# Optimization experiments

Hardware: AMD Instinct MI355X
Metric: run time of the kernel (lower is better)

The kernel has to match this reference:

```python
import jax, jax.numpy as jnp
import numpy as np
from jax import lax

B, L, DIM = 2, 2048, 2048
HK, HV = 16, 32
DK, DV = 128, 128
KCONV = 4
KEY_DIM = HK * DK          # 2048
VAL_DIM = HV * DV          # 4096
CONV_DIM = 2 * KEY_DIM + VAL_DIM  # 8192
EPS = 1e-6


def _l2norm(x, eps=1e-6):
    return x * lax.rsqrt((x * x).sum(-1, keepdims=True) + eps)


def _gated_delta_rule(q, k, v, g, beta):
    # q,k: (B,L,H,DK); v: (B,L,H,DV); g,beta: (B,L,H)
    q = _l2norm(q.astype(jnp.float32)) * (DK ** -0.5)
    k = _l2norm(k.astype(jnp.float32))
    v = v.astype(jnp.float32)
    g = g.astype(jnp.float32)
    beta = beta.astype(jnp.float32)
    # time-major for scan: (L,B,H,...)
    qs = q.transpose(1, 0, 2, 3)
    ks = k.transpose(1, 0, 2, 3)
    vs = v.transpose(1, 0, 2, 3)
    gs = g.transpose(1, 0, 2)
    bs = beta.transpose(1, 0, 2)
    state0 = jnp.zeros((B, HV, DK, DV), jnp.float32)

    def step(state, inp):
        q_t, k_t, v_t, g_t, b_t = inp
        state = state * jnp.exp(g_t)[..., None, None]          # decay
        kv_mem = jnp.einsum('bhk,bhkv->bhv', k_t, state)       # read
        delta = (v_t - kv_mem) * b_t[..., None]                # error-correct
        state = state + jnp.einsum('bhk,bhv->bhkv', k_t, delta)
        out_t = jnp.einsum('bhk,bhkv->bhv', q_t, state)
        return state, out_t

    _, outs = lax.scan(step, state0, (qs, ks, vs, gs, bs))
    return outs.transpose(1, 0, 2, 3)  # (B,L,H,DV)


def setup_inputs() -> dict:
    key = jax.random.key(0)
    ks = jax.random.split(key, 8)
    s = 0.02
    return {
        'x': jax.random.normal(ks[0], (B, L, DIM), jnp.float32),
        'W_qkv': jax.random.normal(ks[1], (CONV_DIM, DIM), jnp.float32) * s,
        'W_z': jax.random.normal(ks[2], (VAL_DIM, DIM), jnp.float32) * s,
        'W_a': jax.random.normal(ks[3], (HV, DIM), jnp.float32) * s,
        'W_b': jax.random.normal(ks[4], (HV, DIM), jnp.float32) * s,
        'conv_w': jax.random.normal(ks[5], (CONV_DIM, 1, KCONV), jnp.float32) * 0.2,
        'A_log': jnp.log(jax.random.uniform(ks[6], (HV,), jnp.float32, 1e-6, 16.0)),
        'dt_bias': jnp.ones((HV,), jnp.float32),
        'norm_weight': jnp.ones((DV,), jnp.float32),
        'W_out': jax.random.normal(ks[7], (DIM, VAL_DIM), jnp.float32) * s,
    }


def reference(x, W_qkv, W_z, W_a, W_b, conv_w, A_log, dt_bias, norm_weight, W_out):
    qkv = x @ W_qkv.T                      # (B,L,CONV_DIM)
    z = x @ W_z.T                          # (B,L,VAL_DIM)
    a = x @ W_a.T                          # (B,L,HV)
    b = x @ W_b.T                          # (B,L,HV)
    # depthwise causal conv1d (left pad K-1)
    h = qkv.transpose(0, 2, 1)             # (B,C,L)
    h = lax.conv_general_dilated(h, conv_w, window_strides=(1,),
                                 padding=[(KCONV - 1, 0)],
                                 dimension_numbers=('NCH', 'OIH', 'NCH'),
                                 feature_group_count=CONV_DIM)
    qkv = jax.nn.silu(h.transpose(0, 2, 1))
    q, k, v = jnp.split(qkv, [KEY_DIM, 2 * KEY_DIM], axis=-1)
    q = q.reshape(B, L, HK, DK)
    k = k.reshape(B, L, HK, DK)
    v = v.reshape(B, L, HV, DV)
    rep = HV // HK
    if rep > 1:
        q = jnp.repeat(q, rep, axis=2)
        k = jnp.repeat(k, rep, axis=2)
    g = -jnp.exp(A_log.astype(jnp.float32)) * jax.nn.softplus(a.astype(jnp.float32) + dt_bias)
    beta = jax.nn.sigmoid(b)
    out = _gated_delta_rule(q, k, v, g, beta)   # (B,L,HV,DV) fp32
    # gated RMSNorm over DV: silu(z) * weight * norm(out)
    var = (out * out).mean(-1, keepdims=True)
    out = out * lax.rsqrt(var + EPS) * norm_weight
    zg = z.reshape(B, L, HV, DV)
    out = out * jax.nn.silu(zg.astype(jnp.float32))
    out = out.astype(x.dtype).reshape(B, L, VAL_DIM)
    return out @ W_out.T
```

## Files before the change

### kernel.cpp

```cpp
#include <hip/hip_runtime.h>
#include <hip/hip_bf16.h>
#include <cstddef>
#include <cstdint>

constexpr int B = 2, L = 2048, DIM = 2048;
constexpr int HK = 16, HV = 32, DK = 128, DV = 128;
constexpr int KEY_DIM = HK * DK;
constexpr int VAL_DIM = HV * DV;
constexpr int CONV_DIM = 2 * KEY_DIM + VAL_DIM;
constexpr int NPROJ = CONV_DIM + VAL_DIM + HV + HV;
constexpr int NPAD  = ((NPROJ + 255) / 256) * 256;
constexpr size_t ROWS = (size_t)B * L;
constexpr float EPS = 1e-6f;
constexpr int CHUNK = 64, NCHUNK = L / CHUNK;
constexpr int NCH_TOT = B * HV * NCHUNK;
constexpr int CONV_LT = 8;
constexpr int CONV_TL = L / CONV_LT;

constexpr size_t OFF_QKV  = 0;
constexpr size_t OFF_Z    = OFF_QKV + ROWS * CONV_DIM * 2;
constexpr size_t OFF_A    = OFF_Z   + ROWS * VAL_DIM * 2;
constexpr size_t OFF_B    = OFF_A   + ROWS * HV * 4;
constexpr size_t OFF_G    = OFF_B   + ROWS * HV * 4;
constexpr size_t OFF_BETA = OFF_G   + ROWS * HV * 4;
constexpr size_t OFF_U    = OFF_BETA + ROWS * HV * 4;
constexpr size_t OFF_WQK  = OFF_U + (size_t)NCH_TOT * CHUNK * DV * 4;
constexpr size_t OFF_HALO = OFF_WQK + (size_t)NCH_TOT * CHUNK * CHUNK * 2;
constexpr size_t WS_NEED_BYTES = OFF_HALO + (size_t)3 * B * CONV_LT * CONV_DIM * 2;
constexpr size_t OFF_WCAT = OFF_U;
constexpr size_t OFF_XB   = OFF_WQK;
constexpr size_t OFF_WOB  = OFF_U;
static_assert((size_t)NPAD * DIM * 2 <= (size_t)NCH_TOT * CHUNK * DV * 4, "Wcat fits U");

__device__ __forceinline__ float bf2f(unsigned short u) {
    union { float f; uint32_t i; } c; c.i = ((uint32_t)u) << 16; return c.f;
}
__device__ __forceinline__ unsigned short f2bf(float f) {
    union { float f; uint32_t u; } c; c.f = f;
    uint32_t u = c.u + 0x7FFFu + ((c.u >> 16) & 1u);
    return (unsigned short)(u >> 16);
}
__device__ __forceinline__ uint32_t pk2(float a, float b) {
    return (uint32_t)f2bf(a) | ((uint32_t)f2bf(b) << 16);
}

typedef __attribute__((ext_vector_type(8))) short bfrag;
typedef __attribute__((ext_vector_type(4))) float ffrag;

__device__ __forceinline__ void gload16(const unsigned short* g, unsigned short* l) {
    __builtin_amdgcn_global_load_lds(
        (const __attribute__((address_space(1))) uint32_t*)g,
        (__attribute__((address_space(3))) uint32_t*)l, 16, 0, 0);
}

__device__ __forceinline__ const float* w_row_multi(int n, const float* Wq, const float* Wz,
                                                    const float* Wa, const float* Wb) {
    if (n < CONV_DIM)                return Wq + (size_t)n * DIM;
    if (n < CONV_DIM + VAL_DIM)      return Wz + (size_t)(n - CONV_DIM) * DIM;
    if (n < CONV_DIM + VAL_DIM + HV) return Wa + (size_t)(n - CONV_DIM - VAL_DIM) * DIM;
    return Wb + (size_t)(n - CONV_DIM - VAL_DIM - HV) * DIM;
}

__global__ __launch_bounds__(256) void cvt_wcat(
    const float* __restrict__ Wq, const float* __restrict__ Wz,
    const float* __restrict__ Wa, const float* __restrict__ Wb,
    unsigned short* __restrict__ dst)
{
    const int r = blockIdx.x;
    const int c = threadIdx.x * 8;
    uint4 o;
    if (r < NPROJ) {
        const float* s = w_row_multi(r, Wq, Wz, Wa, Wb) + c;
        float4 v0 = *(const float4*)s;
        float4 v1 = *(const float4*)(s + 4);
        o = make_uint4(pk2(v0.x, v0.y), pk2(v0.z, v0.w), pk2(v1.x, v1.y), pk2(v1.z, v1.w));
    } else {
        o = make_uint4(0u, 0u, 0u, 0u);
    }
    *(uint4*)&dst[(size_t)r * DIM + c] = o;
}

__global__ __launch_bounds__(256) void cvt_f32bf(const float* __restrict__ src,
                                                 unsigned short* __restrict__ dst, int cols)
{
    const size_t r = blockIdx.x;
    for (int c = threadIdx.x * 8; c < cols; c += 256 * 8) {
        const float* s = src + r * cols + c;
        float4 v0 = *(const float4*)s;
        float4 v1 = *(const float4*)(s + 4);
        *(uint4*)&dst[r * cols + c] =
            make_uint4(pk2(v0.x, v0.y), pk2(v0.z, v0.w), pk2(v1.x, v1.y), pk2(v1.z, v1.w));
    }
}

__device__ __forceinline__ void store_multi(int m, int n, float v,
                                            unsigned short* qkv, unsigned short* z,
                                            float* a, float* b) {
    if (n < CONV_DIM) {
        qkv[(size_t)m * CONV_DIM + n] = f2bf(v);
    } else if (n < CONV_DIM + VAL_DIM) {
        z[(size_t)m * VAL_DIM + (n - CONV_DIM)] = f2bf(v);
    } else if (n < CONV_DIM + VAL_DIM + HV) {
        a[(size_t)m * HV + (n - CONV_DIM - VAL_DIM)] = v;
    } else if (n < NPROJ) {
        b[(size_t)m * HV + (n - CONV_DIM - VAL_DIM - HV)] = v;
    }
}

constexpr int BK = 64;

__global__ __launch_bounds__(512, 2) void gemm_inproj_bf(
    const unsigned short* __restrict__ xb,
    const unsigned short* __restrict__ Wcat,
    unsigned short* __restrict__ qkv, unsigned short* __restrict__ z,
    float* __restrict__ a_out, float* __restrict__ b_out)
{
    extern __shared__ __align__(16) unsigned short lds[];

    constexpr int NBX = NPAD / 256;
    constexpr int NB  = NBX * 16;
    const int id  = blockIdx.x;
    const int swz = (id & 7) * (NB >> 3) + (id >> 3);
    const int bx  = swz >> 4;
    const int by  = swz & 15;
    const int row0 = by * 256;
    const int col0 = bx * 256;

    const int t = threadIdx.x, lane = t & 63, wid = t >> 6;
    const int wr = wid >> 2, wc = wid & 3;
    const int quad = lane >> 4, l16 = lane & 15;

    ffrag acc[8][4];
#pragma unroll
    for (int i = 0; i < 8; ++i)
#pragma unroll
        for (int j = 0; j < 4; ++j) acc[i][j] = (ffrag)0.f;

    const int srow  = t >> 3;
    const int sslot = t & 7;
    const int scol  = ((sslot ^ (srow & 7)) * 8);
    const unsigned short* aS = xb   + (size_t)(row0 + srow) * DIM + scol;
    const unsigned short* bS = Wcat + (size_t)(col0 + srow) * DIM + scol;
    unsigned short* aD0 = lds + (wid * 8) * 64;
    unsigned short* bD0 = lds + 32768 + (wid * 8) * 64;

    const int x7 = l16 & 7;

    auto STAGE = [&](int buf, int k0) {
        unsigned short* aD = aD0 + buf * 16384;
        unsigned short* bD = bD0 + buf * 16384;
#pragma unroll
        for (int j = 0; j < 4; ++j) {
            gload16(aS + (size_t)(j * 64) * DIM + k0, aD + j * 64 * 64);
            gload16(bS + (size_t)(j * 64) * DIM + k0, bD + j * 64 * 64);
        }
    };

    auto COMPUTE = [&](int buf) {
        const unsigned short* A  = lds + buf * 16384;
        const unsigned short* Bm = lds + 32768 + buf * 16384;
#pragma unroll
        for (int kk = 0; kk < 2; ++kk) {
            const int so = ((kk * 4 + quad) ^ x7) * 8;
            bfrag aF[8], bF[4];
#pragma unroll
            for (int m = 0; m < 8; ++m)
                aF[m] = *(const bfrag*)&A[(wr * 128 + m * 16 + l16) * 64 + so];
#pragma unroll
            for (int n = 0; n < 4; ++n)
                bF[n] = *(const bfrag*)&Bm[(wc * 64 + n * 16 + l16) * 64 + so];
#pragma unroll
            for (int m = 0; m < 8; ++m)
#pragma unroll
                for (int n = 0; n < 4; ++n)
                    acc[m][n] = __builtin_amdgcn_mfma_f32_16x16x32_bf16(
                        aF[m], bF[n], acc[m][n], 0, 0, 0);
        }
    };

    STAGE(0, 0);
    __syncthreads();
    for (int kt = 0; kt < DIM / BK; ++kt) {
        if (kt + 1 < DIM / BK) STAGE((kt + 1) & 1, (kt + 1) * BK);
        COMPUTE(kt & 1);
        __syncthreads();
    }

#pragma unroll
    for (int m = 0; m < 8; ++m)
#pragma unroll
        for (int n = 0; n < 4; ++n) {
            int gr = row0 + wr * 128 + m * 16 + quad * 4;
            int gc = col0 + wc * 64 + n * 16 + l16;
#pragma unroll
            for (int reg = 0; reg < 4; ++reg)
                store_multi(gr + reg, gc, acc[m][n][reg], qkv, z, a_out, b_out);
        }
}

__global__ __launch_bounds__(256) void gemm_outproj_bf(
    const unsigned short* __restrict__ A,
    const unsigned short* __restrict__ Wb,
    float* __restrict__ C)
{
    __shared__ __align__(16) unsigned short As[2][128 * BK];
    __shared__ __align__(16) unsigned short Bs[2][128 * BK];

    constexpr int NB = (ROWS / 128) * (DIM / 128);
    const int id  = blockIdx.x;
    const int swz = (id & 7) * (NB >> 3) + (id >> 3);
    const int bx  = swz >> 5;
    const int by  = swz & 31;
    const int row0 = by * 128;
    const int col0 = bx * 128;

    const int t = threadIdx.x, lane = t & 63, wid = t >> 6;
    const int quad = lane >> 4, l16 = lane & 15;
    const int wm = (wid >> 1) * 64, wn = (wid & 1) * 64;

    ffrag acc[4][4];
#pragma unroll
    for (int i = 0; i < 4; ++i)
#pragma unroll
        for (int j = 0; j < 4; ++j) acc[i][j] = (ffrag)0.f;

    const int srow  = t >> 3;
    const int sslot = t & 7;
    const int scol  = ((sslot ^ (srow & 7)) * 8);
    const unsigned short* aS = A  + (size_t)(row0 + srow) * VAL_DIM + scol;
    const unsigned short* bS = Wb + (size_t)(col0 + srow) * VAL_DIM + scol;

    const int aBase = (wm + l16) * BK;
    const int bBase = (wn + l16) * BK;
    const int x7 = l16 & 7;

    auto STAGE = [&](int buf, int k0) {
        unsigned short* aD = &As[buf][(wid * 8) * 64];
        unsigned short* bD = &Bs[buf][(wid * 8) * 64];
#pragma unroll
        for (int j = 0; j < 4; ++j) {
            gload16(aS + (size_t)(j * 32) * VAL_DIM + k0, aD + j * 32 * 64);
            gload16(bS + (size_t)(j * 32) * VAL_DIM + k0, bD + j * 32 * 64);
        }
    };

    auto COMPUTE = [&](int buf) {
#pragma unroll
        for (int kk = 0; kk < 2; ++kk) {
            const int so = ((kk * 4 + quad) ^ x7) * 8;
            bfrag aF[4], bF[4];
#pragma unroll
            for (int mt = 0; mt < 4; ++mt) aF[mt] = *(const bfrag*)&As[buf][aBase + mt * 16 * BK + so];
#pragma unroll
            for (int nt = 0; nt < 4; ++nt) bF[nt] = *(const bfrag*)&Bs[buf][bBase + nt * 16 * BK + so];
#pragma unroll
            for (int mt = 0; mt < 4; ++mt)
#pragma unroll
                for (int nt = 0; nt < 4; ++nt)
                    acc[mt][nt] = __builtin_amdgcn_mfma_f32_16x16x32_bf16(
                        aF[mt], bF[nt], acc[mt][nt], 0, 0, 0);
        }
    };

    STAGE(0, 0);
    __syncthreads();
    for (int kt = 0; kt < VAL_DIM / BK; ++kt) {
        if (kt + 1 < VAL_DIM / BK) STAGE((kt + 1) & 1, (kt + 1) * BK);
        COMPUTE(kt & 1);
        __syncthreads();
    }

#pragma unroll
    for (int mt = 0; mt < 4; ++mt)
#pragma unroll
        for (int nt = 0; nt < 4; ++nt) {
            int gr = row0 + wm + mt * 16 + quad * 4;
            int gc = col0 + wn + nt * 16 + l16;
#pragma unroll
            for (int reg = 0; reg < 4; ++reg)
                C[(size_t)(gr + reg) * DIM + gc] = acc[mt][nt][reg];
        }
}

__global__ __launch_bounds__(256) void conv_halo(const unsigned short* __restrict__ qkv,
                                                 unsigned short* __restrict__ hbuf)
{
    int idx = blockIdx.x * 256 + threadIdx.x;
    int c    = idx & (CONV_DIM - 1);
    int tile = (idx >> 13) & (CONV_LT - 1);
    int b    = idx >> 16;
    int l0 = tile * CONV_TL;
    const unsigned short* p = qkv + (size_t)b * L * CONV_DIM + c;
#pragma unroll
    for (int j = 0; j < 3; ++j) {
        unsigned short v = (tile > 0) ? p[(size_t)(l0 - 3 + j) * CONV_DIM] : (unsigned short)0;
        hbuf[((size_t)j * B * CONV_LT + b * CONV_LT + tile) * CONV_DIM + c] = v;
    }
}

__global__ __launch_bounds__(256) void conv_silu(unsigned short* __restrict__ qkv,
                                                 const float* __restrict__ conv_w,
                                                 const unsigned short* __restrict__ hbuf)
{
    int idx = blockIdx.x * 256 + threadIdx.x;
    int c    = idx & (CONV_DIM - 1);
    int tile = (idx >> 13) & (CONV_LT - 1);
    int b    = idx >> 16;
    const float w0 = conv_w[c * 4 + 0];
    const float w1 = conv_w[c * 4 + 1];
    const float w2 = conv_w[c * 4 + 2];
    const float w3 = conv_w[c * 4 + 3];
    unsigned short* p = qkv + ((size_t)b * L + tile * CONV_TL) * CONV_DIM + c;
    const size_t hb = (size_t)b * CONV_LT + tile;
    float x0 = bf2f(hbuf[((size_t)0 * B * CONV_LT + hb) * CONV_DIM + c]);
    float x1 = bf2f(hbuf[((size_t)1 * B * CONV_LT + hb) * CONV_DIM + c]);
    float x2 = bf2f(hbuf[((size_t)2 * B * CONV_LT + hb) * CONV_DIM + c]);
    for (int l0 = 0; l0 < CONV_TL; l0 += 8) {
        float xv[8];
#pragma unroll
        for (int j = 0; j < 8; ++j) xv[j] = bf2f(p[(size_t)(l0 + j) * CONV_DIM]);
#pragma unroll
        for (int j = 0; j < 8; ++j) {
            float h = w0 * x0 + w1 * x1 + w2 * x2 + w3 * xv[j];
            float s = h / (1.f + __expf(-h));
            p[(size_t)(l0 + j) * CONV_DIM] = f2bf(s);
            x0 = x1; x1 = x2; x2 = xv[j];
        }
    }
}

__global__ __launch_bounds__(256) void normqk(unsigned short* __restrict__ qkv)
{
    int wid  = blockIdx.x * 4 + (threadIdx.x >> 6);
    int lane = threadIdx.x & 63;
    int hk  = wid & 15;
    int sel = (wid >> 4) & 1;
    int row = wid >> 5;
    unsigned short* p = qkv + (size_t)row * CONV_DIM + sel * KEY_DIM + hk * DK;
    float x0 = bf2f(p[lane]), x1 = bf2f(p[lane + 64]);
    float ss = x0 * x0 + x1 * x1;
#pragma unroll
    for (int o = 32; o >= 1; o >>= 1) ss += __shfl_xor(ss, o);
    float sc = rsqrtf(ss + 1e-6f);
    if (sel == 0) sc *= 0.08838834764831845f;
    p[lane]      = f2bf(x0 * sc);
    p[lane + 64] = f2bf(x1 * sc);
}

__global__ __launch_bounds__(256) void gatecoef(const float* __restrict__ a_buf,
                                                const float* __restrict__ b_buf,
                                                const float* __restrict__ A_log,
                                                const float* __restrict__ dt_bias,
                                                float* __restrict__ glog,
                                                float* __restrict__ beta)
{
    int idx = blockIdx.x * blockDim.x + threadIdx.x;
    int h = idx & (HV - 1);
    float av = a_buf[idx];
    float bv = b_buf[idx];
    float x  = av + dt_bias[h];
    float sp = (x > 20.f) ? x : log1pf(__expf(x));
    glog[idx] = -__expf(A_log[h]) * sp;
    beta[idx] = 1.f / (1.f + __expf(-bv));
}


constexpr int RSK  = 136;
constexpr int RST  = 72;
constexpr int RSTD = 68;
constexpr int RSR1 = 260;

constexpr int P1_oKs  = 0;
constexpr int P1_oQs  = P1_oKs + 64 * RSK * 2;
constexpr int P1_oDT  = 0;
constexpr int P1_oAf  = P1_oQs + 64 * RSK * 2;
constexpr int P1_oRHS = P1_oAf + 64 * RST * 2;
constexpr int P1_oG   = P1_oRHS + 64 * RSR1 * 4;
constexpr int P1_oEG  = P1_oG + 256;
constexpr int P1_oBs  = P1_oEG + 256;
constexpr int P1_SMEM = P1_oBs + 256;

__global__ __launch_bounds__(256, 1) void chunk_prep(
    unsigned short* __restrict__ qkv,
    const float* __restrict__ glog,
    const float* __restrict__ beta,
    float* __restrict__ Ubuf,
    unsigned short* __restrict__ Wqkbuf)
{
    extern __shared__ __align__(16) char smem[];
    unsigned short* sKs = (unsigned short*)(smem + P1_oKs);
    unsigned short* sQs = (unsigned short*)(smem + P1_oQs);
    unsigned short* sDT = (unsigned short*)(smem + P1_oDT);
    unsigned short* sAf = (unsigned short*)(smem + P1_oAf);
    float* sRHS = (float*)(smem + P1_oRHS);
    float* sG   = (float*)(smem + P1_oG);
    float* sEG  = (float*)(smem + P1_oEG);
    float* sBs  = (float*)(smem + P1_oBs);

    const int bid = blockIdx.x;
    const int ch = bid & (NCHUNK - 1);
    const int h  = (bid >> 5) & (HV - 1);
    const int bb = bid >> 10;
    const int hk = h >> 1;
    const int t    = threadIdx.x;
    const int w    = t >> 6;
    const int lane = t & 63;
    const int quad = lane >> 4;
    const int l16  = lane & 15;
    const int quad8 = quad * 8;
    const size_t bL = (size_t)bb * L;
    const int l0 = ch * CHUNK;
    const int VOFF = 2 * KEY_DIM + h * DV;

    {
        const int r  = t >> 2;
        const int c0 = (t & 3) * 32;
        const unsigned short* grow = qkv + (bL + l0 + r) * CONV_DIM;
        const unsigned short* gq = grow + hk * DK + c0;
        const unsigned short* gk = grow + KEY_DIM + hk * DK + c0;
#pragma unroll
        for (int u = 0; u < 4; ++u) {
            *(uint4*)&sKs[r * RSK + c0 + 8 * u] = *(const uint4*)(gk + 8 * u);
            *(uint4*)&sQs[r * RSK + c0 + 8 * u] = *(const uint4*)(gq + 8 * u);
        }
        if (t < 64) {
            float gl = glog[(bL + l0 + t) * HV + h];
#pragma unroll
            for (int off = 1; off < 64; off <<= 1) {
                float v = __shfl_up(gl, off, 64);
                if (lane >= off) gl += v;
            }
            sG[t]  = gl;
            sEG[t] = __expf(gl);
            sBs[t] = beta[(bL + l0 + t) * HV + h];
        }
    }
    __syncthreads();

    {
        ffrag accA[4], accW[4];
#pragma unroll
        for (int mt = 0; mt < 4; ++mt) { accA[mt] = (ffrag)0.f; accW[mt] = (ffrag)0.f; }
#pragma unroll
        for (int kk = 0; kk < 4; ++kk) {
            bfrag bf = *(const bfrag*)&sKs[(16 * w + l16) * RSK + 32 * kk + quad8];
#pragma unroll
            for (int mt = 0; mt < 4; ++mt) {
                bfrag ak = *(const bfrag*)&sKs[(16 * mt + l16) * RSK + 32 * kk + quad8];
                bfrag aq = *(const bfrag*)&sQs[(16 * mt + l16) * RSK + 32 * kk + quad8];
                accA[mt] = __builtin_amdgcn_mfma_f32_16x16x32_bf16(ak, bf, accA[mt], 0, 0, 0);
                accW[mt] = __builtin_amdgcn_mfma_f32_16x16x32_bf16(aq, bf, accW[mt], 0, 0, 0);
            }
        }
        const int j = 16 * w + l16;
        const float gj = sG[j];
        unsigned short* Wqp = Wqkbuf + (size_t)bid * (CHUNK * CHUNK);
#pragma unroll
        for (int mt = 0; mt < 4; ++mt)
#pragma unroll
            for (int reg = 0; reg < 4; ++reg) {
                int i = 16 * mt + quad * 4 + reg;
                float sc = __expf(sG[i] - gj);
                sAf[i * RST + j] = f2bf((j < i) ? sBs[i] * sc * accA[mt][reg] : 0.f);
                Wqp[i * CHUNK + j] = f2bf((j <= i) ? sc * accW[mt][reg] : 0.f);
            }
    }

    {
        const int r  = t >> 2;
        const int c0 = (t & 3) * 32;
        const float be  = sBs[r];
        const float beg = be * sEG[r];
        const unsigned short* gv = qkv + (bL + l0 + r) * CONV_DIM + VOFF + c0;
#pragma unroll
        for (int u = 0; u < 4; ++u) {
            uint4 vv = *(const uint4*)(gv + 8 * u);
            const unsigned short* vp = (const unsigned short*)&vv;
#pragma unroll
            for (int e = 0; e < 8; ++e)
                sRHS[r * RSR1 + c0 + 8 * u + e] = be * bf2f(vp[e]);
        }
#pragma unroll
        for (int u = 0; u < 4; ++u)
#pragma unroll
            for (int e = 0; e < 8; ++e)
                sRHS[r * RSR1 + 128 + c0 + 8 * u + e] =
                    beg * bf2f(sKs[r * RSK + c0 + 8 * u + e]);
    }
    __syncthreads();

    for (int u = t; u < 256 * RSTD / 2; u += 256) ((uint32_t*)sDT)[u] = 0;

    float* Up = Ubuf + (size_t)bid * (CHUNK * DV);
    for (int sb = 0; sb < 4; ++sb) {
        const int sb16 = 16 * sb;
        if (sb > 0) {
            const int kbn = (sb + 1) >> 1;
            ffrag c16[4];
#pragma unroll
            for (int nt = 0; nt < 4; ++nt) c16[nt] = (ffrag)0.f;
            for (int kb = 0; kb < kbn; ++kb) {
                bfrag af = *(const bfrag*)&sAf[(sb16 + l16) * RST + 32 * kb + quad8];
#pragma unroll
                for (int nt = 0; nt < 4; ++nt) {
                    bfrag bf = *(const bfrag*)&sDT[(64 * w + 16 * nt + l16) * RSTD + 32 * kb + quad8];
                    c16[nt] = __builtin_amdgcn_mfma_f32_16x16x32_bf16(af, bf, c16[nt], 0, 0, 0);
                }
            }
#pragma unroll
            for (int nt = 0; nt < 4; ++nt)
#pragma unroll
                for (int reg = 0; reg < 4; ++reg)
                    sRHS[(sb16 + quad * 4 + reg) * RSR1 + 64 * w + 16 * nt + l16] -= c16[nt][reg];
        }
        __syncthreads();
        {
            const int c = t;
            float d16[16];
#pragma unroll
            for (int e = 0; e < 16; ++e) {
                const int i = sb16 + e;
                float acc = sRHS[i * RSR1 + c];
#pragma unroll
                for (int f = 0; f < 16; ++f)
                    if (f < e) acc -= bf2f(sAf[i * RST + sb16 + f]) * d16[f];
                d16[e] = acc;
            }
#pragma unroll
            for (int e = 0; e < 16; e += 2)
                *(uint32_t*)&sDT[c * RSTD + sb16 + e] = pk2(d16[e], d16[e + 1]);
            if (c < 128) {
                float* up = Up + c;
#pragma unroll
                for (int e = 0; e < 16; ++e) up[(size_t)(sb16 + e) * DV] = d16[e];
            } else {
                unsigned short* wp = qkv + (bL + l0 + sb16) * CONV_DIM + VOFF + (c - 128);
#pragma unroll
                for (int e = 0; e < 16; ++e) wp[(size_t)e * CONV_DIM] = f2bf(-d16[e]);
            }
        }
        __syncthreads();
    }
}

constexpr int P2_oSTb = 0;
constexpr int P2_oWk  = P2_oSTb + 128 * RSK * 2;
constexpr int P2_oQs  = P2_oWk + 64 * RSK * 2;
constexpr int P2_oKT  = P2_oQs + 64 * RSK * 2;
constexpr int P2_oWqk = P2_oKT + 128 * RST * 2;
constexpr int P2_oDT  = P2_oWqk + 64 * RST * 2;
constexpr int P2_oDdT = P2_oDT + 128 * RST * 2;
constexpr int P2_oEG  = P2_oDdT + 128 * RST * 2;
constexpr int P2_oEGd = P2_oEG + 256;
constexpr int P2_oNW  = P2_oEGd + 256;
constexpr int P2_SMEM = P2_oNW + 512;

__global__ __launch_bounds__(256, 1) void chunk_scan2(
    const unsigned short* __restrict__ qkv,
    const float* __restrict__ glog,
    const float* __restrict__ Ubuf,
    const unsigned short* __restrict__ Wqkbuf,
    unsigned short* __restrict__ z_io,
    const float* __restrict__ norm_w)
{
    extern __shared__ __align__(16) char smem[];
    unsigned short* sSTb = (unsigned short*)(smem + P2_oSTb);
    unsigned short* sWk  = (unsigned short*)(smem + P2_oWk);
    unsigned short* sQs  = (unsigned short*)(smem + P2_oQs);
    unsigned short* sKT  = (unsigned short*)(smem + P2_oKT);
    unsigned short* sWqk = (unsigned short*)(smem + P2_oWqk);
    unsigned short* sDT  = (unsigned short*)(smem + P2_oDT);
    unsigned short* sDdT = (unsigned short*)(smem + P2_oDdT);
    float* sEG  = (float*)(smem + P2_oEG);
    float* sEGd = (float*)(smem + P2_oEGd);
    float* sNW  = (float*)(smem + P2_oNW);

    const int bb = blockIdx.x >> 5;
    const int h  = blockIdx.x & (HV - 1);
    const int hk = h >> 1;
    const int t    = threadIdx.x;
    const int w    = t >> 6;
    const int lane = t & 63;
    const int quad = lane >> 4;
    const int l16  = lane & 15;
    const int quad8 = quad * 8;
    const size_t bL = (size_t)bb * L;
    const int VOFF = 2 * KEY_DIM + h * DV;
    const size_t chbase0 = ((size_t)bb * HV + h) * NCHUNK;

    const int r  = t >> 2;
    const int c0 = (t & 3) * 32;
    const int cw = (t & 3) * 16;

    ffrag accS[2][8];
#pragma unroll
    for (int mt = 0; mt < 2; ++mt)
#pragma unroll
        for (int nt = 0; nt < 8; ++nt) accS[mt][nt] = (ffrag)0.f;

    for (int u = t; u < 64 * RSK; u += 256) ((uint32_t*)sSTb)[u] = 0;
    if (t < 128) sNW[t] = norm_w[t];

    uint4 pQ[4], pK[4], pWk[4], pWqk2[2];
    float pGl;

    auto PF = [&](int ch) {
        const int l0p = ch * CHUNK;
        const unsigned short* grow = qkv + (bL + l0p + r) * CONV_DIM;
        const unsigned short* gq = grow + hk * DK + c0;
        const unsigned short* gk = grow + KEY_DIM + hk * DK + c0;
        const unsigned short* gw = grow + VOFF + c0;
#pragma unroll
        for (int u = 0; u < 4; ++u) {
            pQ[u]  = *(const uint4*)(gq + 8 * u);
            pK[u]  = *(const uint4*)(gk + 8 * u);
            pWk[u] = *(const uint4*)(gw + 8 * u);
        }
        const unsigned short* qp = Wqkbuf + (chbase0 + ch) * (CHUNK * CHUNK) + r * CHUNK + cw;
        pWqk2[0] = *(const uint4*)qp;
        pWqk2[1] = *(const uint4*)(qp + 8);
        pGl = glog[(bL + l0p + (t & 63)) * HV + h];
    };

    PF(0);

    for (int ch = 0; ch < NCHUNK; ++ch) {
        const int l0 = ch * CHUNK;
        const size_t cb = chbase0 + ch;
        __syncthreads();

        ffrag accD[4][2];
        {
            const float* up = Ubuf + cb * (CHUNK * DV) + (size_t)(quad * 4) * DV + 32 * w + l16;
#pragma unroll
            for (int mt = 0; mt < 4; ++mt)
#pragma unroll
                for (int nt = 0; nt < 2; ++nt)
#pragma unroll
                    for (int reg = 0; reg < 4; ++reg)
                        accD[mt][nt][reg] = up[(size_t)(16 * mt + reg) * DV + 16 * nt];
        }
        unsigned short pz[8][4];
        {
            const unsigned short* zp =
                z_io + (bL + l0 + 16 * w + quad * 4) * (size_t)VAL_DIM + h * DV + l16;
#pragma unroll
            for (int nt = 0; nt < 8; ++nt)
#pragma unroll
                for (int reg = 0; reg < 4; ++reg)
                    pz[nt][reg] = zp[(size_t)reg * VAL_DIM + 16 * nt];
        }

#pragma unroll
        for (int u = 0; u < 4; ++u) {
            *(uint4*)&sQs[r * RSK + c0 + 8 * u] = pQ[u];
            *(uint4*)&sWk[r * RSK + c0 + 8 * u] = pWk[u];
            const unsigned short* kp = (const unsigned short*)&pK[u];
#pragma unroll
            for (int e = 0; e < 8; ++e) {
                const int c = c0 + 8 * u + e;
                sKT[c * RST + ((((r >> 3) ^ (c >> 3)) & 7) << 3) + (r & 7)] = kp[e];
            }
        }
        *(uint4*)&sWqk[r * RST + cw]     = pWqk2[0];
        *(uint4*)&sWqk[r * RST + cw + 8] = pWqk2[1];

        {
            float gl = pGl;
            if (t < 64) {
#pragma unroll
                for (int off = 1; off < 64; off <<= 1) {
                    float v = __shfl_up(gl, off, 64);
                    if (lane >= off) gl += v;
                }
                float gc = __shfl(gl, 63, 64);
                sEG[t]  = __expf(gl);
                sEGd[t] = __expf(gc - gl);
            }
        }

        if (ch + 1 < NCHUNK) PF(ch + 1);
        __syncthreads();

#pragma unroll
        for (int kk = 0; kk < 4; ++kk) {
            bfrag b0 = *(const bfrag*)&sSTb[(32 * w + l16) * RSK + 32 * kk + quad8];
            bfrag b1 = *(const bfrag*)&sSTb[(32 * w + 16 + l16) * RSK + 32 * kk + quad8];
#pragma unroll
            for (int mt = 0; mt < 4; ++mt) {
                bfrag af = *(const bfrag*)&sWk[(16 * mt + l16) * RSK + 32 * kk + quad8];
                accD[mt][0] = __builtin_amdgcn_mfma_f32_16x16x32_bf16(af, b0, accD[mt][0], 0, 0, 0);
                accD[mt][1] = __builtin_amdgcn_mfma_f32_16x16x32_bf16(af, b1, accD[mt][1], 0, 0, 0);
            }
        }

#pragma unroll
        for (int mt = 0; mt < 4; ++mt) {
            const int i0 = 16 * mt + quad * 4;
            const float e0 = sEGd[i0], e1 = sEGd[i0 + 1], e2 = sEGd[i0 + 2], e3 = sEGd[i0 + 3];
#pragma unroll
            for (int nt = 0; nt < 2; ++nt) {
                const int dv = 32 * w + 16 * nt + l16;
                const float d0 = accD[mt][nt][0], d1 = accD[mt][nt][1];
                const float d2 = accD[mt][nt][2], d3 = accD[mt][nt][3];
                *(uint32_t*)&sDT[dv * RST + i0]      = pk2(d0, d1);
                *(uint32_t*)&sDT[dv * RST + i0 + 2]  = pk2(d2, d3);
                *(uint32_t*)&sDdT[dv * RST + i0]     = pk2(d0 * e0, d1 * e1);
                *(uint32_t*)&sDdT[dv * RST + i0 + 2] = pk2(d2 * e2, d3 * e3);
            }
        }
        __syncthreads();

        {
            ffrag accO[8];
#pragma unroll
            for (int nt = 0; nt < 8; ++nt) accO[nt] = (ffrag)0.f;
#pragma unroll
            for (int kk = 0; kk < 4; ++kk) {
                bfrag af = *(const bfrag*)&sQs[(16 * w + l16) * RSK + 32 * kk + quad8];
#pragma unroll
                for (int nt = 0; nt < 8; ++nt) {
                    bfrag bf = *(const bfrag*)&sSTb[(16 * nt + l16) * RSK + 32 * kk + quad8];
                    accO[nt] = __builtin_amdgcn_mfma_f32_16x16x32_bf16(af, bf, accO[nt], 0, 0, 0);
                }
            }
#pragma unroll
            for (int nt = 0; nt < 8; ++nt)
#pragma unroll
                for (int reg = 0; reg < 4; ++reg)
                    accO[nt][reg] *= sEG[16 * w + quad * 4 + reg];
#pragma unroll
            for (int kk = 0; kk < 2; ++kk) {
                bfrag af = *(const bfrag*)&sWqk[(16 * w + l16) * RST + 32 * kk + quad8];
#pragma unroll
                for (int nt = 0; nt < 8; ++nt) {
                    bfrag bf = *(const bfrag*)&sDT[(16 * nt + l16) * RST + 32 * kk + quad8];
                    accO[nt] = __builtin_amdgcn_mfma_f32_16x16x32_bf16(af, bf, accO[nt], 0, 0, 0);
                }
            }
            float inv[4];
#pragma unroll
            for (int reg = 0; reg < 4; ++reg) {
                float p = 0.f;
#pragma unroll
                for (int nt = 0; nt < 8; ++nt) p += accO[nt][reg] * accO[nt][reg];
#pragma unroll
                for (int m = 1; m < 16; m <<= 1) p += __shfl_xor(p, m, 64);
                inv[reg] = rsqrtf(p * (1.f / 128.f) + EPS);
            }
            unsigned short* zw =
                z_io + (bL + l0 + 16 * w + quad * 4) * (size_t)VAL_DIM + h * DV + l16;
#pragma unroll
            for (int nt = 0; nt < 8; ++nt) {
                const float nwv = sNW[16 * nt + l16];
#pragma unroll
                for (int reg = 0; reg < 4; ++reg) {
                    float zv = bf2f(pz[nt][reg]);
                    float y = accO[nt][reg] * inv[reg] * nwv * (zv / (1.f + __expf(-zv)));
                    zw[(size_t)reg * VAL_DIM + 16 * nt] = f2bf(y);
                }
            }

            const float eGc = sEG[63];
#pragma unroll
            for (int mt = 0; mt < 2; ++mt)
#pragma unroll
                for (int nt = 0; nt < 8; ++nt)
#pragma unroll
                    for (int reg = 0; reg < 4; ++reg) accS[mt][nt][reg] *= eGc;
#pragma unroll
            for (int kk = 0; kk < 2; ++kk) {
                bfrag a0 = *(const bfrag*)&sDdT[(32 * w + l16) * RST + 32 * kk + quad8];
                bfrag a1 = *(const bfrag*)&sDdT[(32 * w + 16 + l16) * RST + 32 * kk + quad8];
#pragma unroll
                for (int nt = 0; nt < 8; ++nt) {
                    const int ck = 16 * nt + l16;
                    bfrag bk = *(const bfrag*)&sKT[ck * RST +
                                 ((((4 * kk + quad) ^ (ck >> 3)) & 7) << 3)];
                    accS[0][nt] = __builtin_amdgcn_mfma_f32_16x16x32_bf16(a0, bk, accS[0][nt], 0, 0, 0);
                    accS[1][nt] = __builtin_amdgcn_mfma_f32_16x16x32_bf16(a1, bk, accS[1][nt], 0, 0, 0);
                }
            }
        }
        __syncthreads();

#pragma unroll
        for (int mt = 0; mt < 2; ++mt)
#pragma unroll
            for (int nt = 0; nt < 8; ++nt)
#pragma unroll
                for (int reg = 0; reg < 4; ++reg)
                    sSTb[(32 * w + 16 * mt + quad * 4 + reg) * RSK + 16 * nt + l16] =
                        f2bf(accS[mt][nt][reg]);
    }
}

extern "C" void kernel_launch(void* const* d_in, const int* in_sizes, int n_in,
                              void* d_out, int out_size, void* d_ws, size_t ws_size,
                              hipStream_t stream)
{
    const float* x        = (const float*)d_in[0];
    const float* W_qkv    = (const float*)d_in[1];
    const float* W_z      = (const float*)d_in[2];
    const float* W_a      = (const float*)d_in[3];
    const float* W_b      = (const float*)d_in[4];
    const float* conv_w   = (const float*)d_in[5];
    const float* A_log    = (const float*)d_in[6];
    const float* dt_bias  = (const float*)d_in[7];
    const float* norm_w   = (const float*)d_in[8];
    const float* W_out    = (const float*)d_in[9];
    float* out = (float*)d_out;
    char*  ws  = (char*)d_ws;

    if (ws_size < WS_NEED_BYTES) return;

    unsigned short* qkv = (unsigned short*)(ws + OFF_QKV);
    unsigned short* z   = (unsigned short*)(ws + OFF_Z);
    float* a    = (float*)(ws + OFF_A);
    float* bbuf = (float*)(ws + OFF_B);
    float* gl   = (float*)(ws + OFF_G);
    float* beta = (float*)(ws + OFF_BETA);
    float* Ubuf = (float*)(ws + OFF_U);
    unsigned short* Wqkbuf = (unsigned short*)(ws + OFF_WQK);
    unsigned short* hbuf   = (unsigned short*)(ws + OFF_HALO);
    unsigned short* Wcat   = (unsigned short*)(ws + OFF_WCAT);
    unsigned short* xb     = (unsigned short*)(ws + OFF_XB);
    unsigned short* Wob    = (unsigned short*)(ws + OFF_WOB);

    static bool attr_set = false;
    if (!attr_set) {
        (void)hipFuncSetAttribute((const void*)chunk_prep,
                                  hipFuncAttributeMaxDynamicSharedMemorySize, P1_SMEM);
        (void)hipFuncSetAttribute((const void*)chunk_scan2,
                                  hipFuncAttributeMaxDynamicSharedMemorySize, P2_SMEM);
        (void)hipFuncSetAttribute((const void*)gemm_inproj_bf,
                                  hipFuncAttributeMaxDynamicSharedMemorySize, 131072);
        attr_set = true;
    }

    cvt_wcat<<<NPAD, 256, 0, stream>>>(W_qkv, W_z, W_a, W_b, Wcat);
    cvt_f32bf<<<(int)ROWS, 256, 0, stream>>>(x, xb, DIM);
    gemm_inproj_bf<<<(NPAD / 256) * 16, 512, 131072, stream>>>(xb, Wcat, qkv, z, a, bbuf);
    conv_halo<<<(B * CONV_LT * CONV_DIM) / 256, 256, 0, stream>>>(qkv, hbuf);
    conv_silu<<<(B * CONV_LT * CONV_DIM) / 256, 256, 0, stream>>>(qkv, conv_w, hbuf);
    normqk<<<(B * L * 2 * HK) / 4, 256, 0, stream>>>(qkv);
    gatecoef<<<(B * L * HV) / 256, 256, 0, stream>>>(a, bbuf, A_log, dt_bias, gl, beta);
    chunk_prep<<<NCH_TOT, 256, P1_SMEM, stream>>>(qkv, gl, beta, Ubuf, Wqkbuf);
    chunk_scan2<<<B * HV, 256, P2_SMEM, stream>>>(qkv, gl, Ubuf, Wqkbuf, z, norm_w);
    cvt_f32bf<<<DIM, 256, 0, stream>>>(W_out, Wob, VAL_DIM);
    gemm_outproj_bf<<<(ROWS / 128) * (DIM / 128), 256, 0, stream>>>(z, Wob, out);
}
```

Before: 989.8 us.

## Double chunk_scan2 threads to 512 and split per-chunk work across eight waves

The sequential chunk scan kernel now runs with 512 threads (8 waves) instead of 256. Each wave owns 16 rows of the state and half of the output columns for a 16-row group. RMSNorm partial sums are exchanged through a small shared buffer. The goal is to raise latency hiding and MFMA throughput in this kernel, which has only 64 blocks and is the serial bottleneck. The cost is an extra barrier and shared-memory exchange per chunk, and per-wave MFMA chains that are now shorter.

```diff
diff --git a/kernel.cpp b/kernel.cpp
--- a/kernel.cpp
+++ b/kernel.cpp
@@ -553,9 +553,10 @@
 constexpr int P2_oEG  = P2_oDdT + 128 * RST * 2;
 constexpr int P2_oEGd = P2_oEG + 256;
 constexpr int P2_oNW  = P2_oEGd + 256;
-constexpr int P2_SMEM = P2_oNW + 512;
-
-__global__ __launch_bounds__(256, 1) void chunk_scan2(
+constexpr int P2_oP   = P2_oNW + 512;
+constexpr int P2_SMEM = P2_oP + 512;
+
+__global__ __launch_bounds__(512, 1) void chunk_scan2(
     const unsigned short* __restrict__ qkv,
     const float* __restrict__ glog,
     const float* __restrict__ Ubuf,
@@ -574,6 +575,7 @@
     float* sEG  = (float*)(smem + P2_oEG);
     float* sEGd = (float*)(smem + P2_oEGd);
     float* sNW  = (float*)(smem + P2_oNW);
+    float* sP   = (float*)(smem + P2_oP);
 
     const int bb = blockIdx.x >> 5;
     const int h  = blockIdx.x & (HV - 1);
@@ -584,24 +586,24 @@
     const int quad = lane >> 4;
     const int l16  = lane & 15;
     const int quad8 = quad * 8;
+    const int rg = w >> 1;
+    const int dh = w & 1;
     const size_t bL = (size_t)bb * L;
     const int VOFF = 2 * KEY_DIM + h * DV;
     const size_t chbase0 = ((size_t)bb * HV + h) * NCHUNK;
 
-    const int r  = t >> 2;
-    const int c0 = (t & 3) * 32;
-    const int cw = (t & 3) * 16;
-
-    ffrag accS[2][8];
-#pragma unroll
-    for (int mt = 0; mt < 2; ++mt)
-#pragma unroll
-        for (int nt = 0; nt < 8; ++nt) accS[mt][nt] = (ffrag)0.f;
-
-    for (int u = t; u < 64 * RSK; u += 256) ((uint32_t*)sSTb)[u] = 0;
+    const int r  = t >> 3;
+    const int c0 = (t & 7) * 16;
+    const int cw = (t & 7) * 8;
+
+    ffrag accS[8];
+#pragma unroll
+    for (int nt = 0; nt < 8; ++nt) accS[nt] = (ffrag)0.f;
+
+    for (int u = t; u < 64 * RSK; u += 512) ((uint32_t*)sSTb)[u] = 0;
     if (t < 128) sNW[t] = norm_w[t];
 
-    uint4 pQ[4], pK[4], pWk[4], pWqk2[2];
+    uint4 pQ[2], pK[2], pWk[2], pWqk;
     float pGl;
 
     auto PF = [&](int ch) {
@@ -611,14 +613,12 @@
         const unsigned short* gk = grow + KEY_DIM + hk * DK + c0;
         const unsigned short* gw = grow + VOFF + c0;
 #pragma unroll
-        for (int u = 0; u < 4; ++u) {
+        for (int u = 0; u < 2; ++u) {
             pQ[u]  = *(const uint4*)(gq + 8 * u);
             pK[u]  = *(const uint4*)(gk + 8 * u);
             pWk[u] = *(const uint4*)(gw + 8 * u);
         }
-        const unsigned short* qp = Wqkbuf + (chbase0 + ch) * (CHUNK * CHUNK) + r * CHUNK + cw;
-        pWqk2[0] = *(const uint4*)qp;
-        pWqk2[1] = *(const uint4*)(qp + 8);
+        pWqk = *(const uint4*)(Wqkbuf + (chbase0 + ch) * (CHUNK * CHUNK) + r * CHUNK + cw);
         pGl = glog[(bL + l0p + (t & 63)) * HV + h];
     };
 
@@ -629,30 +629,28 @@
         const size_t cb = chbase0 + ch;
         __syncthreads();
 
-        ffrag accD[4][2];
+        ffrag accD[4];
         {
-            const float* up = Ubuf + cb * (CHUNK * DV) + (size_t)(quad * 4) * DV + 32 * w + l16;
+            const float* up = Ubuf + cb * (CHUNK * DV) + (size_t)(quad * 4) * DV + 16 * w + l16;
 #pragma unroll
             for (int mt = 0; mt < 4; ++mt)
 #pragma unroll
-                for (int nt = 0; nt < 2; ++nt)
-#pragma unroll
-                    for (int reg = 0; reg < 4; ++reg)
-                        accD[mt][nt][reg] = up[(size_t)(16 * mt + reg) * DV + 16 * nt];
-        }
-        unsigned short pz[8][4];
+                for (int reg = 0; reg < 4; ++reg)
+                    accD[mt][reg] = up[(size_t)(16 * mt + reg) * DV];
+        }
+        unsigned short pz[4][4];
         {
             const unsigned short* zp =
-                z_io + (bL + l0 + 16 * w + quad * 4) * (size_t)VAL_DIM + h * DV + l16;
-#pragma unroll
-            for (int nt = 0; nt < 8; ++nt)
+                z_io + (bL + l0 + 16 * rg + quad * 4) * (size_t)VAL_DIM + h * DV + 64 * dh + l16;
+#pragma unroll
+            for (int nt = 0; nt < 4; ++nt)
 #pragma unroll
                 for (int reg = 0; reg < 4; ++reg)
                     pz[nt][reg] = zp[(size_t)reg * VAL_DIM + 16 * nt];
         }
 
 #pragma unroll
-        for (int u = 0; u < 4; ++u) {
+        for (int u = 0; u < 2; ++u) {
             *(uint4*)&sQs[r * RSK + c0 + 8 * u] = pQ[u];
             *(uint4*)&sWk[r * RSK + c0 + 8 * u] = pWk[u];
             const unsigned short* kp = (const unsigned short*)&pK[u];
@@ -662,8 +660,7 @@
                 sKT[c * RST + ((((r >> 3) ^ (c >> 3)) & 7) << 3) + (r & 7)] = kp[e];
             }
         }
-        *(uint4*)&sWqk[r * RST + cw]     = pWqk2[0];
-        *(uint4*)&sWqk[r * RST + cw + 8] = pWqk2[1];
+        *(uint4*)&sWqk[r * RST + cw] = pWqk;
 
         {
             float gl = pGl;
@@ -684,25 +681,22 @@
 
 #pragma unroll
         for (int kk = 0; kk < 4; ++kk) {
-            bfrag b0 = *(const bfrag*)&sSTb[(32 * w + l16) * RSK + 32 * kk + quad8];
-            bfrag b1 = *(const bfrag*)&sSTb[(32 * w + 16 + l16) * RSK + 32 * kk + quad8];
+            bfrag b0 = *(const bfrag*)&sSTb[(16 * w + l16) * RSK + 32 * kk + quad8];
 #pragma unroll
             for (int mt = 0; mt < 4; ++mt) {
                 bfrag af = *(const bfrag*)&sWk[(16 * mt + l16) * RSK + 32 * kk + quad8];
-                accD[mt][0] = __builtin_amdgcn_mfma_f32_16x16x32_bf16(af, b0, accD[mt][0], 0, 0, 0);
-                accD[mt][1] = __builtin_amdgcn_mfma_f32_16x16x32_bf16(af, b1, accD[mt][1], 0, 0, 0);
-            }
-        }
-
-#pragma unroll
-        for (int mt = 0; mt < 4; ++mt) {
-            const int i0 = 16 * mt + quad * 4;
-            const float e0 = sEGd[i0], e1 = sEGd[i0 + 1], e2 = sEGd[i0 + 2], e3 = sEGd[i0 + 3];
-#pragma unroll
-            for (int nt = 0; nt < 2; ++nt) {
-                const int dv = 32 * w + 16 * nt + l16;
-                const float d0 = accD[mt][nt][0], d1 = accD[mt][nt][1];
-                const float d2 = accD[mt][nt][2], d3 = accD[mt][nt][3];
+                accD[mt] = __builtin_amdgcn_mfma_f32_16x16x32_bf16(af, b0, accD[mt], 0, 0, 0);
+            }
+        }
+
+        {
+            const int dv = 16 * w + l16;
+#pragma unroll
+            for (int mt = 0; mt < 4; ++mt) {
+                const int i0 = 16 * mt + quad * 4;
+                const float e0 = sEGd[i0], e1 = sEGd[i0 + 1], e2 = sEGd[i0 + 2], e3 = sEGd[i0 + 3];
+                const float d0 = accD[mt][0], d1 = accD[mt][1];
+                const float d2 = accD[mt][2], d3 = accD[mt][3];
                 *(uint32_t*)&sDT[dv * RST + i0]      = pk2(d0, d1);
                 *(uint32_t*)&sDT[dv * RST + i0 + 2]  = pk2(d2, d3);
                 *(uint32_t*)&sDdT[dv * RST + i0]     = pk2(d0 * e0, d1 * e1);
@@ -711,48 +705,80 @@
         }
         __syncthreads();
 
+        ffrag accO[4];
+#pragma unroll
+        for (int nt = 0; nt < 4; ++nt) accO[nt] = (ffrag)0.f;
+#pragma unroll
+        for (int kk = 0; kk < 4; ++kk) {
+            bfrag af = *(const bfrag*)&sQs[(16 * rg + l16) * RSK + 32 * kk + quad8];
+#pragma unroll
+            for (int nt = 0; nt < 4; ++nt) {
+                bfrag bf = *(const bfrag*)&sSTb[(64 * dh + 16 * nt + l16) * RSK + 32 * kk + quad8];
+                accO[nt] = __builtin_amdgcn_mfma_f32_16x16x32_bf16(af, bf, accO[nt], 0, 0, 0);
+            }
+        }
+#pragma unroll
+        for (int nt = 0; nt < 4; ++nt)
+#pragma unroll
+            for (int reg = 0; reg < 4; ++reg)
+                accO[nt][reg] *= sEG[16 * rg + quad * 4 + reg];
+#pragma unroll
+        for (int kk = 0; kk < 2; ++kk) {
+            bfrag af = *(const bfrag*)&sWqk[(16 * rg + l16) * RST + 32 * kk + quad8];
+#pragma unroll
+            for (int nt = 0; nt < 4; ++nt) {
+                bfrag bf = *(const bfrag*)&sDT[(64 * dh + 16 * nt + l16) * RST + 32 * kk + quad8];
+                accO[nt] = __builtin_amdgcn_mfma_f32_16x16x32_bf16(af, bf, accO[nt], 0, 0, 0);
+            }
+        }
+
+        float p4[4];
+#pragma unroll
+        for (int reg = 0; reg < 4; ++reg) {
+            float p = 0.f;
+#pragma unroll
+            for (int nt = 0; nt < 4; ++nt) p += accO[nt][reg] * accO[nt][reg];
+#pragma unroll
+            for (int m = 1; m < 16; m <<= 1) p += __shfl_xor(p, m, 64);
+            p4[reg] = p;
+        }
+        if (l16 == 0) {
+#pragma unroll
+            for (int reg = 0; reg < 4; ++reg) sP[w * 16 + quad * 4 + reg] = p4[reg];
+        }
+
         {
-            ffrag accO[8];
-#pragma unroll
-            for (int nt = 0; nt < 8; ++nt) accO[nt] = (ffrag)0.f;
-#pragma unroll
-            for (int kk = 0; kk < 4; ++kk) {
-                bfrag af = *(const bfrag*)&sQs[(16 * w + l16) * RSK + 32 * kk + quad8];
+            const float eGc = sEG[63];
+#pragma unroll
+            for (int nt = 0; nt < 8; ++nt)
+#pragma unroll
+                for (int reg = 0; reg < 4; ++reg) accS[nt][reg] *= eGc;
+#pragma unroll
+            for (int kk = 0; kk < 2; ++kk) {
+                bfrag a0 = *(const bfrag*)&sDdT[(16 * w + l16) * RST + 32 * kk + quad8];
 #pragma unroll
                 for (int nt = 0; nt < 8; ++nt) {
-                    bfrag bf = *(const bfrag*)&sSTb[(16 * nt + l16) * RSK + 32 * kk + quad8];
-                    accO[nt] = __builtin_amdgcn_mfma_f32_16x16x32_bf16(af, bf, accO[nt], 0, 0, 0);
+                    const int ck = 16 * nt + l16;
+                    bfrag bk = *(const bfrag*)&sKT[ck * RST +
+                                 ((((4 * kk + quad) ^ (ck >> 3)) & 7) << 3)];
+                    accS[nt] = __builtin_amdgcn_mfma_f32_16x16x32_bf16(a0, bk, accS[nt], 0, 0, 0);
                 }
             }
-#pragma unroll
-            for (int nt = 0; nt < 8; ++nt)
-#pragma unroll
-                for (int reg = 0; reg < 4; ++reg)
-                    accO[nt][reg] *= sEG[16 * w + quad * 4 + reg];
-#pragma unroll
-            for (int kk = 0; kk < 2; ++kk) {
-                bfrag af = *(const bfrag*)&sWqk[(16 * w + l16) * RST + 32 * kk + quad8];
-#pragma unroll
-                for (int nt = 0; nt < 8; ++nt) {
-                    bfrag bf = *(const bfrag*)&sDT[(16 * nt + l16) * RST + 32 * kk + quad8];
-                    accO[nt] = __builtin_amdgcn_mfma_f32_16x16x32_bf16(af, bf, accO[nt], 0, 0, 0);
-                }
-            }
+        }
+        __syncthreads();
+
+        {
             float inv[4];
 #pragma unroll
             for (int reg = 0; reg < 4; ++reg) {
-                float p = 0.f;
-#pragma unroll
-                for (int nt = 0; nt < 8; ++nt) p += accO[nt][reg] * accO[nt][reg];
-#pragma unroll
-                for (int m = 1; m < 16; m <<= 1) p += __shfl_xor(p, m, 64);
-                inv[reg] = rsqrtf(p * (1.f / 128.f) + EPS);
+                float pp = p4[reg] + sP[(w ^ 1) * 16 + quad * 4 + reg];
+                inv[reg] = rsqrtf(pp * (1.f / 128.f) + EPS);
             }
             unsigned short* zw =
-                z_io + (bL + l0 + 16 * w + quad * 4) * (size_t)VAL_DIM + h * DV + l16;
-#pragma unroll
-            for (int nt = 0; nt < 8; ++nt) {
-                const float nwv = sNW[16 * nt + l16];
+                z_io + (bL + l0 + 16 * rg + quad * 4) * (size_t)VAL_DIM + h * DV + 64 * dh + l16;
+#pragma unroll
+            for (int nt = 0; nt < 4; ++nt) {
+                const float nwv = sNW[64 * dh + 16 * nt + l16];
 #pragma unroll
                 for (int reg = 0; reg < 4; ++reg) {
                     float zv = bf2f(pz[nt][reg]);
@@ -760,38 +786,13 @@
                     zw[(size_t)reg * VAL_DIM + 16 * nt] = f2bf(y);
                 }
             }
-
-            const float eGc = sEG[63];
-#pragma unroll
-            for (int mt = 0; mt < 2; ++mt)
-#pragma unroll
-                for (int nt = 0; nt < 8; ++nt)
-#pragma unroll
-                    for (int reg = 0; reg < 4; ++reg) accS[mt][nt][reg] *= eGc;
-#pragma unroll
-            for (int kk = 0; kk < 2; ++kk) {
-                bfrag a0 = *(const bfrag*)&sDdT[(32 * w + l16) * RST + 32 * kk + quad8];
-                bfrag a1 = *(const bfrag*)&sDdT[(32 * w + 16 + l16) * RST + 32 * kk + quad8];
-#pragma unroll
-                for (int nt = 0; nt < 8; ++nt) {
-                    const int ck = 16 * nt + l16;
-                    bfrag bk = *(const bfrag*)&sKT[ck * RST +
-                                 ((((4 * kk + quad) ^ (ck >> 3)) & 7) << 3)];
-                    accS[0][nt] = __builtin_amdgcn_mfma_f32_16x16x32_bf16(a0, bk, accS[0][nt], 0, 0, 0);
-                    accS[1][nt] = __builtin_amdgcn_mfma_f32_16x16x32_bf16(a1, bk, accS[1][nt], 0, 0, 0);
-                }
-            }
-        }
-        __syncthreads();
-
-#pragma unroll
-        for (int mt = 0; mt < 2; ++mt)
-#pragma unroll
-            for (int nt = 0; nt < 8; ++nt)
-#pragma unroll
-                for (int reg = 0; reg < 4; ++reg)
-                    sSTb[(32 * w + 16 * mt + quad * 4 + reg) * RSK + 16 * nt + l16] =
-                        f2bf(accS[mt][nt][reg]);
+        }
+
+#pragma unroll
+        for (int nt = 0; nt < 8; ++nt)
+#pragma unroll
+            for (int reg = 0; reg < 4; ++reg)
+                sSTb[(16 * w + quad * 4 + reg) * RSK + 16 * nt + l16] = f2bf(accS[nt][reg]);
     }
 }
 
@@ -846,7 +847,7 @@
     normqk<<<(B * L * 2 * HK) / 4, 256, 0, stream>>>(qkv);
     gatecoef<<<(B * L * HV) / 256, 256, 0, stream>>>(a, bbuf, A_log, dt_bias, gl, beta);
     chunk_prep<<<NCH_TOT, 256, P1_SMEM, stream>>>(qkv, gl, beta, Ubuf, Wqkbuf);
-    chunk_scan2<<<B * HV, 256, P2_SMEM, stream>>>(qkv, gl, Ubuf, Wqkbuf, z, norm_w);
+    chunk_scan2<<<B * HV, 512, P2_SMEM, stream>>>(qkv, gl, Ubuf, Wqkbuf, z, norm_w);
     cvt_f32bf<<<DIM, 256, 0, stream>>>(W_out, Wob, VAL_DIM);
     gemm_outproj_bf<<<(ROWS / 128) * (DIM / 128), 256, 0, stream>>>(z, Wob, out);
 }
```

After: 966.3 us. 2.4% less time.
